# Kernel optimization log

Hardware: AMD Instinct MI355X
Metric: run time of the kernel (lower is better)

## Reference

```python
import jax, jax.numpy as jnp
import numpy as np

KK_THRESHOLD = 1000.0

def setup_inputs() -> dict:
    key = jax.random.key(0)
    k1, k2 = jax.random.split(key)
    x = jax.random.normal(k1, (8192, 4096), dtype=jnp.float32)
    # kernel initialized Uniform(-0.1, 0.1) as in the original layer
    kernel = jax.random.uniform(k2, (4096, 4096), dtype=jnp.float32, minval=-0.1, maxval=0.1)
    bias = jnp.zeros((4096,), dtype=jnp.float32)
    nmk = jnp.float32(1.0)
    kk = jnp.float32(1.0)  # < 1000 -> soft tanh quantization branch
    return {"x": x, "kernel": kernel, "bias": bias, "nmk": nmk, "kk": kk}

def reference(x, kernel, bias, nmk, kk):
    def soft(_):
        # training-time soft binarization: tanh(kk * W)
        return nmk * jnp.matmul(x, jnp.tanh(kernel * kk)) + bias
    def hard(_):
        # fully binarized: sign(W)
        return nmk * jnp.matmul(x, jnp.sign(kernel)) + bias
    return jax.lax.cond(kk < KK_THRESHOLD, soft, hard, operand=None)
```

## Files before the change

kernel.cpp:

```cpp
#include <hip/hip_runtime.h>
#include <hip/hip_bf16.h>
#include <stdint.h>

typedef __bf16 bf16x8 __attribute__((ext_vector_type(8)));
typedef float f32x4 __attribute__((ext_vector_type(4)));
typedef unsigned int u32;
typedef __attribute__((address_space(1))) const u32 g_u32;
typedef __attribute__((address_space(3))) u32 l_u32;

__device__ __forceinline__ unsigned short f32_bf16_rne(float f) {
    unsigned u = __float_as_uint(f);
    u += 0x7FFFu + ((u >> 16) & 1u);
    return (unsigned short)(u >> 16);
}

__device__ __forceinline__ float fast_tanh(float z) {
    return 1.0f - 2.0f / (1.0f + __expf(2.0f * z));
}

__device__ __forceinline__ void lds16(const void* g, void* l) {
    __builtin_amdgcn_global_load_lds((g_u32*)g, (l_u32*)l, 16, 0, 0);
}

__global__ __launch_bounds__(256) void prep(
    const float* __restrict__ x, unsigned short* __restrict__ xb, int n8,
    const float* __restrict__ W, unsigned short* __restrict__ Wt,
    const float* __restrict__ kk_p, int K, int N, int qbx, int qblocks)
{
    const int t = threadIdx.x;
    if ((int)blockIdx.x < qblocks) {
        __shared__ unsigned short tileT[64][66];
        const float kk = *kk_p;
        const bool soft = kk < 1000.0f;
        const int nb = (blockIdx.x % qbx) * 64;
        const int kb = (blockIdx.x / qbx) * 64;
#pragma unroll
        for (int j = 0; j < 4; ++j) {
            const int r  = j * 16 + (t >> 4);
            const int c4 = (t & 15) * 4;
            float4 w = *(const float4*)&W[(size_t)(kb + r) * N + nb + c4];
            float q0, q1, q2, q3;
            if (soft) {
                q0 = fast_tanh(w.x * kk); q1 = fast_tanh(w.y * kk);
                q2 = fast_tanh(w.z * kk); q3 = fast_tanh(w.w * kk);
            } else {
                q0 = (w.x > 0.f) ? 1.f : (w.x < 0.f ? -1.f : 0.f);
                q1 = (w.y > 0.f) ? 1.f : (w.y < 0.f ? -1.f : 0.f);
                q2 = (w.z > 0.f) ? 1.f : (w.z < 0.f ? -1.f : 0.f);
                q3 = (w.w > 0.f) ? 1.f : (w.w < 0.f ? -1.f : 0.f);
            }
            tileT[c4 + 0][r] = f32_bf16_rne(q0);
            tileT[c4 + 1][r] = f32_bf16_rne(q1);
            tileT[c4 + 2][r] = f32_bf16_rne(q2);
            tileT[c4 + 3][r] = f32_bf16_rne(q3);
        }
        __syncthreads();
#pragma unroll
        for (int j = 0; j < 2; ++j) {
            const int n = j * 32 + (t >> 3);
            const int c = (t & 7) * 8;
            uint4 v;
            v.x = *(const u32*)&tileT[n][c + 0];
            v.y = *(const u32*)&tileT[n][c + 2];
            v.z = *(const u32*)&tileT[n][c + 4];
            v.w = *(const u32*)&tileT[n][c + 6];
            *(uint4*)&Wt[(size_t)(nb + n) * K + kb + c] = v;
        }
    } else {
        const int i = ((int)blockIdx.x - qblocks) * 256 + t;
        if (i >= n8) return;
        const float4* p = (const float4*)x + (size_t)i * 2;
        float4 a = p[0];
        float4 b = p[1];
        union { unsigned short u[8]; uint4 v; } o;
        o.u[0] = f32_bf16_rne(a.x); o.u[1] = f32_bf16_rne(a.y);
        o.u[2] = f32_bf16_rne(a.z); o.u[3] = f32_bf16_rne(a.w);
        o.u[4] = f32_bf16_rne(b.x); o.u[5] = f32_bf16_rne(b.y);
        o.u[6] = f32_bf16_rne(b.z); o.u[7] = f32_bf16_rne(b.w);
        *((uint4*)xb + i) = o.v;
    }
}

__global__ __launch_bounds__(512, 2) void gemm_bf16_256(
    const unsigned short* __restrict__ A,
    const unsigned short* __restrict__ Bt,
    const float* __restrict__ bias,
    const float* __restrict__ nmk_p,
    float* __restrict__ C,
    int M, int N, int K)
{
    __shared__ __align__(16) char lds[131072];

    const int tid  = threadIdx.x;
    const int wave = tid >> 6;
    const int lane = tid & 63;
    const int wr = wave >> 2;
    const int wc = wave & 3;

    const int nbx = N >> 8;
    const int nwg = (int)gridDim.x;
    int id = (int)blockIdx.x;
    {
        const int xcd = id & 7, lid = id >> 3;
        const int q8 = nwg >> 3, r8 = nwg & 7;
        id = (xcd < r8 ? xcd * (q8 + 1) : r8 * (q8 + 1) + (xcd - r8) * q8) + lid;
    }
    const int mTile = (id / nbx) << 8;
    const int nTile = (id % nbx) << 8;

    const size_t Kb = (size_t)K * 2;
    const char* pA[2];
    const char* pB[2];
#pragma unroll
    for (int q = 0; q < 2; ++q) {
        const int s  = (wave * 2 + q) * 64 + lane;
        const int g  = s >> 6;
        const int r4 = (s >> 2) & 15;
        const int c4 = (s & 3) ^ ((r4 >> 1) & 3);
        const int row = ((g >> 1) << 4) + r4;
        const int cb  = (((g & 1) << 2) + c4) << 4;
        pA[q] = (const char*)A  + (size_t)(mTile + row) * Kb + cb;
        pB[q] = (const char*)Bt + (size_t)(nTile + row) * Kb + cb;
    }
    const size_t HSTEP = (size_t)128 * Kb;
    const int w2k = wave * 2048;

    const int laneoff = ((lane & 15) << 6)
                      + ((((lane >> 4) ^ (((lane & 15) >> 1) & 3))) << 4);

    f32x4 acc[8][4] = {};
    const int NT = K >> 6;

#define STG_A(buf, t, h) do {                                                  \
    char* _d = lds + (buf) * 65536 + (h) * 16384 + w2k;                        \
    lds16(pA[0] + (size_t)(h) * HSTEP + (size_t)(t) * 128, _d);                \
    lds16(pA[1] + (size_t)(h) * HSTEP + (size_t)(t) * 128, _d + 1024);         \
} while (0)
#define STG_B(buf, t, h) do {                                                  \
    char* _d = lds + 32768 + (buf) * 65536 + (h) * 16384 + w2k;                \
    lds16(pB[0] + (size_t)(h) * HSTEP + (size_t)(t) * 128, _d);                \
    lds16(pB[1] + (size_t)(h) * HSTEP + (size_t)(t) * 128, _d + 1024);         \
} while (0)
#define LDA(dst, buf, mi, ks) dst = *(const bf16x8*)(lds + (buf) * 65536       \
        + ((wr * 8 + (mi)) * 2048) + (ks) * 1024 + laneoff)
#define LDB(dst, buf, ni, ks) dst = *(const bf16x8*)(lds + 32768               \
        + (buf) * 65536 + ((wc * 4 + (ni)) * 2048) + (ks) * 1024 + laneoff)
#define BAR() __builtin_amdgcn_s_barrier()
#define LGKM0() asm volatile("s_waitcnt lgkmcnt(0)" ::: "memory")
#define MFMA_Q(p)                                                              \
    __builtin_amdgcn_s_setprio(1);                                             \
    { _Pragma("unroll")                                                        \
      for (int ii = 0; ii < 2; ++ii) {                                         \
        _Pragma("unroll")                                                      \
        for (int ni = 0; ni < 4; ++ni) {                                       \
          _Pragma("unroll")                                                    \
          for (int ks = 0; ks < 2; ++ks)                                       \
            acc[2 * (p) + ii][ni] = __builtin_amdgcn_mfma_f32_16x16x32_bf16(   \
                af[ii][ks], bf[ni][ks], acc[2 * (p) + ii][ni], 0, 0, 0);       \
        } } }                                                                  \
    __builtin_amdgcn_s_setprio(0)

    STG_A(0, 0, 0); STG_A(0, 0, 1);
    STG_B(0, 0, 0); STG_B(0, 0, 1);
    STG_B(1, 1, 0); STG_B(1, 1, 1);
    asm volatile("s_waitcnt vmcnt(4)" ::: "memory");
    BAR();

    bf16x8 af[2][2], bf[4][2];

    for (int t = 0; t < NT; ++t) {
        const int buf = t & 1;
        const int tA = (t + 1 < NT) ? (t + 1) : 0;
        int tB = t + 2; if (tB >= NT) tB -= NT;

        LDB(bf[0][0], buf, 0, 0); LDB(bf[0][1], buf, 0, 1);
        LDB(bf[1][0], buf, 1, 0); LDB(bf[1][1], buf, 1, 1);
        LDB(bf[2][0], buf, 2, 0); LDB(bf[2][1], buf, 2, 1);
        LDB(bf[3][0], buf, 3, 0); LDB(bf[3][1], buf, 3, 1);
        LDA(af[0][0], buf, 0, 0); LDA(af[0][1], buf, 0, 1);
        LDA(af[1][0], buf, 1, 0); LDA(af[1][1], buf, 1, 1);
        STG_A(buf ^ 1, tA, 0);
        BAR(); LGKM0();
        MFMA_Q(0);
        BAR();

        LDA(af[0][0], buf, 2, 0); LDA(af[0][1], buf, 2, 1);
        LDA(af[1][0], buf, 3, 0); LDA(af[1][1], buf, 3, 1);
        STG_A(buf ^ 1, tA, 1);
        BAR(); LGKM0();
        MFMA_Q(1);
        BAR();

        LDA(af[0][0], buf, 4, 0); LDA(af[0][1], buf, 4, 1);
        LDA(af[1][0], buf, 5, 0); LDA(af[1][1], buf, 5, 1);
        STG_B(buf, tB, 0);
        BAR(); LGKM0();
        MFMA_Q(2);
        BAR();

        LDA(af[0][0], buf, 6, 0); LDA(af[0][1], buf, 6, 1);
        LDA(af[1][0], buf, 7, 0); LDA(af[1][1], buf, 7, 1);
        STG_B(buf, tB, 1);
        asm volatile("s_waitcnt vmcnt(4)" ::: "memory");
        BAR(); LGKM0();
        MFMA_Q(3);
        BAR();
    }

    const float nmk = *nmk_p;
    const int l15 = lane & 15, lh = lane >> 4;
    float bn[4];
#pragma unroll
    for (int ni = 0; ni < 4; ++ni) bn[ni] = bias[nTile + wc * 64 + ni * 16 + l15];

#pragma unroll
    for (int mi = 0; mi < 8; ++mi) {
        const int rbase = mTile + wr * 128 + mi * 16 + lh * 4;
#pragma unroll
        for (int ni = 0; ni < 4; ++ni) {
            const int col = nTile + wc * 64 + ni * 16 + l15;
#pragma unroll
            for (int reg = 0; reg < 4; ++reg) {
                C[(size_t)(rbase + reg) * N + col] = nmk * acc[mi][ni][reg] + bn[ni];
            }
        }
    }
#undef STG_A
#undef STG_B
#undef LDA
#undef LDB
#undef BAR
#undef LGKM0
#undef MFMA_Q
}

__global__ void fallback_gemm(const float* __restrict__ x, const float* __restrict__ W,
                              const float* __restrict__ bias, const float* __restrict__ nmk_p,
                              const float* __restrict__ kk_p, float* __restrict__ C,
                              int M, int N, int K) {
    __shared__ float At[16][17];
    __shared__ float Bq[16][17];
    const int tx = threadIdx.x, ty = threadIdx.y;
    const int n = blockIdx.x * 16 + tx;
    const int m = blockIdx.y * 16 + ty;
    const float kk = *kk_p;
    const bool soft = kk < 1000.f;
    float acc = 0.f;
    for (int k0 = 0; k0 < K; k0 += 16) {
        At[ty][tx] = x[(size_t)m * K + k0 + tx];
        float w = W[(size_t)(k0 + ty) * N + n];
        Bq[ty][tx] = soft ? tanhf(w * kk) : (w > 0.f ? 1.f : (w < 0.f ? -1.f : 0.f));
        __syncthreads();
#pragma unroll
        for (int kk2 = 0; kk2 < 16; ++kk2) acc += At[ty][kk2] * Bq[kk2][tx];
        __syncthreads();
    }
    C[(size_t)m * N + n] = (*nmk_p) * acc + bias[n];
}

extern "C" void kernel_launch(void* const* d_in, const int* in_sizes, int n_in,
                              void* d_out, int out_size, void* d_ws, size_t ws_size,
                              hipStream_t stream) {
    const float* x    = (const float*)d_in[0];
    const float* W    = (const float*)d_in[1];
    const float* bias = (const float*)d_in[2];
    const float* nmk  = (const float*)d_in[3];
    const float* kk   = (const float*)d_in[4];
    float* out = (float*)d_out;

    const int N = in_sizes[2];
    const int K = in_sizes[1] / N;
    const int M = in_sizes[0] / K;

    const size_t need = ((size_t)M * K + (size_t)N * K) * sizeof(unsigned short);
    const bool shapes_ok = (M % 256 == 0) && (N % 256 == 0) && (K % 64 == 0) &&
                           (K >= 128) && ((M * K) % 2048 == 0);

    if (ws_size >= need && shapes_ok) {
        unsigned short* xb = (unsigned short*)d_ws;
        unsigned short* Wt = xb + (size_t)M * K;

        const int n8 = (M * K) / 8;
        const int qbx = N / 64;
        const int qblocks = qbx * (K / 64);
        const int cblocks = (n8 + 255) / 256;
        prep<<<qblocks + cblocks, 256, 0, stream>>>(x, xb, n8, W, Wt, kk, K, N, qbx, qblocks);

        const int nwg = (M / 256) * (N / 256);
        gemm_bf16_256<<<nwg, 512, 0, stream>>>(xb, Wt, bias, nmk, out, M, N, K);
    } else {
        dim3 fg(N / 16, M / 16);
        fallback_gemm<<<fg, dim3(16, 16), 0, stream>>>(x, W, bias, nmk, kk, out, M, N, K);
    }
}
```

Measured before the change: 486.9 us.

## Switch GEMM to 32x32x16 MFMA tiles and split prep into separate kernels

The GEMM inner loop now uses 32x32x16 bf16 MFMA instructions with 16-wide accumulators instead of 16x16x32. This cuts the phases per K-step from four to two and changes the LDS fragment addressing and epilogue row mapping to match. The larger MFMA is meant to get more math per LDS read and fewer barriers, at the cost of a different register layout and larger staging batches per phase. The fused prep kernel is also split into separate x-conversion and weight-quantization kernels, with the x conversion reworked to 4 floats per thread and two segments per block.

New measurement: 524.8 us. 1.08x slower.

```diff
diff --git a/kernel.cpp b/kernel.cpp
--- a/kernel.cpp
+++ b/kernel.cpp
@@ -3,7 +3,7 @@
 #include <stdint.h>
 
 typedef __bf16 bf16x8 __attribute__((ext_vector_type(8)));
-typedef float f32x4 __attribute__((ext_vector_type(4)));
+typedef float f32x16 __attribute__((ext_vector_type(16)));
 typedef unsigned int u32;
 typedef __attribute__((address_space(1))) const u32 g_u32;
 typedef __attribute__((address_space(3))) u32 l_u32;
@@ -22,62 +22,65 @@
     __builtin_amdgcn_global_load_lds((g_u32*)g, (l_u32*)l, 16, 0, 0);
 }
 
-__global__ __launch_bounds__(256) void prep(
-    const float* __restrict__ x, unsigned short* __restrict__ xb, int n8,
+__global__ __launch_bounds__(256) void prep_w(
     const float* __restrict__ W, unsigned short* __restrict__ Wt,
-    const float* __restrict__ kk_p, int K, int N, int qbx, int qblocks)
+    const float* __restrict__ kk_p, int K, int N, int qbx)
 {
     const int t = threadIdx.x;
-    if ((int)blockIdx.x < qblocks) {
-        __shared__ unsigned short tileT[64][66];
-        const float kk = *kk_p;
-        const bool soft = kk < 1000.0f;
-        const int nb = (blockIdx.x % qbx) * 64;
-        const int kb = (blockIdx.x / qbx) * 64;
-#pragma unroll
-        for (int j = 0; j < 4; ++j) {
-            const int r  = j * 16 + (t >> 4);
-            const int c4 = (t & 15) * 4;
-            float4 w = *(const float4*)&W[(size_t)(kb + r) * N + nb + c4];
-            float q0, q1, q2, q3;
-            if (soft) {
-                q0 = fast_tanh(w.x * kk); q1 = fast_tanh(w.y * kk);
-                q2 = fast_tanh(w.z * kk); q3 = fast_tanh(w.w * kk);
-            } else {
-                q0 = (w.x > 0.f) ? 1.f : (w.x < 0.f ? -1.f : 0.f);
-                q1 = (w.y > 0.f) ? 1.f : (w.y < 0.f ? -1.f : 0.f);
-                q2 = (w.z > 0.f) ? 1.f : (w.z < 0.f ? -1.f : 0.f);
-                q3 = (w.w > 0.f) ? 1.f : (w.w < 0.f ? -1.f : 0.f);
-            }
-            tileT[c4 + 0][r] = f32_bf16_rne(q0);
-            tileT[c4 + 1][r] = f32_bf16_rne(q1);
-            tileT[c4 + 2][r] = f32_bf16_rne(q2);
-            tileT[c4 + 3][r] = f32_bf16_rne(q3);
+    __shared__ unsigned short tileT[64][66];
+    const float kk = *kk_p;
+    const bool soft = kk < 1000.0f;
+    const int nb = (blockIdx.x % qbx) * 64;
+    const int kb = (blockIdx.x / qbx) * 64;
+#pragma unroll
+    for (int j = 0; j < 4; ++j) {
+        const int r  = j * 16 + (t >> 4);
+        const int c4 = (t & 15) * 4;
+        float4 w = *(const float4*)&W[(size_t)(kb + r) * N + nb + c4];
+        float q0, q1, q2, q3;
+        if (soft) {
+            q0 = fast_tanh(w.x * kk); q1 = fast_tanh(w.y * kk);
+            q2 = fast_tanh(w.z * kk); q3 = fast_tanh(w.w * kk);
+        } else {
+            q0 = (w.x > 0.f) ? 1.f : (w.x < 0.f ? -1.f : 0.f);
+            q1 = (w.y > 0.f) ? 1.f : (w.y < 0.f ? -1.f : 0.f);
+            q2 = (w.z > 0.f) ? 1.f : (w.z < 0.f ? -1.f : 0.f);
+            q3 = (w.w > 0.f) ? 1.f : (w.w < 0.f ? -1.f : 0.f);
         }
-        __syncthreads();
-#pragma unroll
-        for (int j = 0; j < 2; ++j) {
-            const int n = j * 32 + (t >> 3);
-            const int c = (t & 7) * 8;
-            uint4 v;
-            v.x = *(const u32*)&tileT[n][c + 0];
-            v.y = *(const u32*)&tileT[n][c + 2];
-            v.z = *(const u32*)&tileT[n][c + 4];
-            v.w = *(const u32*)&tileT[n][c + 6];
-            *(uint4*)&Wt[(size_t)(nb + n) * K + kb + c] = v;
+        tileT[c4 + 0][r] = f32_bf16_rne(q0);
+        tileT[c4 + 1][r] = f32_bf16_rne(q1);
+        tileT[c4 + 2][r] = f32_bf16_rne(q2);
+        tileT[c4 + 3][r] = f32_bf16_rne(q3);
+    }
+    __syncthreads();
+#pragma unroll
+    for (int j = 0; j < 2; ++j) {
+        const int n = j * 32 + (t >> 3);
+        const int c = (t & 7) * 8;
+        uint4 v;
+        v.x = *(const u32*)&tileT[n][c + 0];
+        v.y = *(const u32*)&tileT[n][c + 2];
+        v.z = *(const u32*)&tileT[n][c + 4];
+        v.w = *(const u32*)&tileT[n][c + 6];
+        *(uint4*)&Wt[(size_t)(nb + n) * K + kb + c] = v;
+    }
+}
+
+__global__ __launch_bounds__(256) void prep_x(
+    const float* __restrict__ x, unsigned short* __restrict__ xb, int nfloat)
+{
+    const int base = (int)blockIdx.x * 2048;
+    const int t = threadIdx.x;
+#pragma unroll
+    for (int seg = 0; seg < 2; ++seg) {
+        const int i = base + seg * 1024 + t * 4;
+        if (i < nfloat) {
+            float4 a = *(const float4*)(x + i);
+            u32 lo = (u32)f32_bf16_rne(a.x) | ((u32)f32_bf16_rne(a.y) << 16);
+            u32 hi = (u32)f32_bf16_rne(a.z) | ((u32)f32_bf16_rne(a.w) << 16);
+            uint2 o; o.x = lo; o.y = hi;
+            *(uint2*)(xb + i) = o;
         }
-    } else {
-        const int i = ((int)blockIdx.x - qblocks) * 256 + t;
-        if (i >= n8) return;
-        const float4* p = (const float4*)x + (size_t)i * 2;
-        float4 a = p[0];
-        float4 b = p[1];
-        union { unsigned short u[8]; uint4 v; } o;
-        o.u[0] = f32_bf16_rne(a.x); o.u[1] = f32_bf16_rne(a.y);
-        o.u[2] = f32_bf16_rne(a.z); o.u[3] = f32_bf16_rne(a.w);
-        o.u[4] = f32_bf16_rne(b.x); o.u[5] = f32_bf16_rne(b.y);
-        o.u[6] = f32_bf16_rne(b.z); o.u[7] = f32_bf16_rne(b.w);
-        *((uint4*)xb + i) = o.v;
     }
 }
 
@@ -125,10 +128,15 @@
     const size_t HSTEP = (size_t)128 * Kb;
     const int w2k = wave * 2048;
 
-    const int laneoff = ((lane & 15) << 6)
-                      + ((((lane >> 4) ^ (((lane & 15) >> 1) & 3))) << 4);
-
-    f32x4 acc[8][4] = {};
+    const int lrow = lane & 31, lr4 = lrow & 15, lg = lrow >> 4, lhi = lane >> 5;
+    const int swz = (lr4 >> 1) & 3;
+    int loff[4];
+#pragma unroll
+    for (int s = 0; s < 4; ++s)
+        loff[s] = lg * 2048 + (s >> 1) * 1024 + lr4 * 64
+                + (((((s & 1) << 1) | lhi) ^ swz) << 4);
+
+    f32x16 acc[4][2] = {};
     const int NT = K >> 6;
 
 #define STG_A(buf, t, h) do {                                                  \
@@ -141,10 +149,10 @@
     lds16(pB[0] + (size_t)(h) * HSTEP + (size_t)(t) * 128, _d);                \
     lds16(pB[1] + (size_t)(h) * HSTEP + (size_t)(t) * 128, _d + 1024);         \
 } while (0)
-#define LDA(dst, buf, mi, ks) dst = *(const bf16x8*)(lds + (buf) * 65536       \
-        + ((wr * 8 + (mi)) * 2048) + (ks) * 1024 + laneoff)
-#define LDB(dst, buf, ni, ks) dst = *(const bf16x8*)(lds + 32768               \
-        + (buf) * 65536 + ((wc * 4 + (ni)) * 2048) + (ks) * 1024 + laneoff)
+#define LDA32(dst, buf, mi, s) dst = *(const bf16x8*)(lds + (buf) * 65536      \
+        + wr * 16384 + (mi) * 4096 + loff[s])
+#define LDB32(dst, buf, ni, s) dst = *(const bf16x8*)(lds + 32768              \
+        + (buf) * 65536 + wc * 8192 + (ni) * 4096 + loff[s])
 #define BAR() __builtin_amdgcn_s_barrier()
 #define LGKM0() asm volatile("s_waitcnt lgkmcnt(0)" ::: "memory")
 #define MFMA_Q(p)                                                              \
@@ -152,11 +160,11 @@
     { _Pragma("unroll")                                                        \
       for (int ii = 0; ii < 2; ++ii) {                                         \
         _Pragma("unroll")                                                      \
-        for (int ni = 0; ni < 4; ++ni) {                                       \
+        for (int ni = 0; ni < 2; ++ni) {                                       \
           _Pragma("unroll")                                                    \
-          for (int ks = 0; ks < 2; ++ks)                                       \
-            acc[2 * (p) + ii][ni] = __builtin_amdgcn_mfma_f32_16x16x32_bf16(   \
-                af[ii][ks], bf[ni][ks], acc[2 * (p) + ii][ni], 0, 0, 0);       \
+          for (int s = 0; s < 4; ++s)                                          \
+            acc[2 * (p) + ii][ni] = __builtin_amdgcn_mfma_f32_32x32x16_bf16(   \
+                af[ii][s], bf[ni][s], acc[2 * (p) + ii][ni], 0, 0, 0);         \
         } } }                                                                  \
     __builtin_amdgcn_s_setprio(0)
 
@@ -166,69 +174,61 @@
     asm volatile("s_waitcnt vmcnt(4)" ::: "memory");
     BAR();
 
-    bf16x8 af[2][2], bf[4][2];
+    bf16x8 af[2][4], bf[2][4];
 
     for (int t = 0; t < NT; ++t) {
         const int buf = t & 1;
         const int tA = (t + 1 < NT) ? (t + 1) : 0;
         int tB = t + 2; if (tB >= NT) tB -= NT;
 
-        LDB(bf[0][0], buf, 0, 0); LDB(bf[0][1], buf, 0, 1);
-        LDB(bf[1][0], buf, 1, 0); LDB(bf[1][1], buf, 1, 1);
-        LDB(bf[2][0], buf, 2, 0); LDB(bf[2][1], buf, 2, 1);
-        LDB(bf[3][0], buf, 3, 0); LDB(bf[3][1], buf, 3, 1);
-        LDA(af[0][0], buf, 0, 0); LDA(af[0][1], buf, 0, 1);
-        LDA(af[1][0], buf, 1, 0); LDA(af[1][1], buf, 1, 1);
+        LDB32(bf[0][0], buf, 0, 0); LDB32(bf[0][1], buf, 0, 1);
+        LDB32(bf[0][2], buf, 0, 2); LDB32(bf[0][3], buf, 0, 3);
+        LDB32(bf[1][0], buf, 1, 0); LDB32(bf[1][1], buf, 1, 1);
+        LDB32(bf[1][2], buf, 1, 2); LDB32(bf[1][3], buf, 1, 3);
+        LDA32(af[0][0], buf, 0, 0); LDA32(af[0][1], buf, 0, 1);
+        LDA32(af[0][2], buf, 0, 2); LDA32(af[0][3], buf, 0, 3);
+        LDA32(af[1][0], buf, 1, 0); LDA32(af[1][1], buf, 1, 1);
+        LDA32(af[1][2], buf, 1, 2); LDA32(af[1][3], buf, 1, 3);
         STG_A(buf ^ 1, tA, 0);
+        STG_A(buf ^ 1, tA, 1);
         BAR(); LGKM0();
         MFMA_Q(0);
         BAR();
 
-        LDA(af[0][0], buf, 2, 0); LDA(af[0][1], buf, 2, 1);
-        LDA(af[1][0], buf, 3, 0); LDA(af[1][1], buf, 3, 1);
-        STG_A(buf ^ 1, tA, 1);
+        LDA32(af[0][0], buf, 2, 0); LDA32(af[0][1], buf, 2, 1);
+        LDA32(af[0][2], buf, 2, 2); LDA32(af[0][3], buf, 2, 3);
+        LDA32(af[1][0], buf, 3, 0); LDA32(af[1][1], buf, 3, 1);
+        LDA32(af[1][2], buf, 3, 2); LDA32(af[1][3], buf, 3, 3);
+        STG_B(buf, tB, 0);
+        STG_B(buf, tB, 1);
         BAR(); LGKM0();
         MFMA_Q(1);
+        asm volatile("s_waitcnt vmcnt(4)" ::: "memory");
         BAR();
-
-        LDA(af[0][0], buf, 4, 0); LDA(af[0][1], buf, 4, 1);
-        LDA(af[1][0], buf, 5, 0); LDA(af[1][1], buf, 5, 1);
-        STG_B(buf, tB, 0);
-        BAR(); LGKM0();
-        MFMA_Q(2);
-        BAR();
-
-        LDA(af[0][0], buf, 6, 0); LDA(af[0][1], buf, 6, 1);
-        LDA(af[1][0], buf, 7, 0); LDA(af[1][1], buf, 7, 1);
-        STG_B(buf, tB, 1);
-        asm volatile("s_waitcnt vmcnt(4)" ::: "memory");
-        BAR(); LGKM0();
-        MFMA_Q(3);
-        BAR();
     }
 
     const float nmk = *nmk_p;
-    const int l15 = lane & 15, lh = lane >> 4;
-    float bn[4];
-#pragma unroll
-    for (int ni = 0; ni < 4; ++ni) bn[ni] = bias[nTile + wc * 64 + ni * 16 + l15];
-
-#pragma unroll
-    for (int mi = 0; mi < 8; ++mi) {
-        const int rbase = mTile + wr * 128 + mi * 16 + lh * 4;
-#pragma unroll
-        for (int ni = 0; ni < 4; ++ni) {
-            const int col = nTile + wc * 64 + ni * 16 + l15;
-#pragma unroll
-            for (int reg = 0; reg < 4; ++reg) {
-                C[(size_t)(rbase + reg) * N + col] = nmk * acc[mi][ni][reg] + bn[ni];
+    float bn[2];
+#pragma unroll
+    for (int ni = 0; ni < 2; ++ni) bn[ni] = bias[nTile + wc * 64 + ni * 32 + lrow];
+
+#pragma unroll
+    for (int mi = 0; mi < 4; ++mi) {
+        const int rbase = mTile + wr * 128 + mi * 32 + 4 * lhi;
+#pragma unroll
+        for (int ni = 0; ni < 2; ++ni) {
+            const int col = nTile + wc * 64 + ni * 32 + lrow;
+#pragma unroll
+            for (int reg = 0; reg < 16; ++reg) {
+                const int row = rbase + (reg & 3) + 8 * (reg >> 2);
+                C[(size_t)row * N + col] = nmk * acc[mi][ni][reg] + bn[ni];
             }
         }
     }
 #undef STG_A
 #undef STG_B
-#undef LDA
-#undef LDB
+#undef LDA32
+#undef LDB32
 #undef BAR
 #undef LGKM0
 #undef MFMA_Q
@@ -280,11 +280,13 @@
         unsigned short* xb = (unsigned short*)d_ws;
         unsigned short* Wt = xb + (size_t)M * K;
 
-        const int n8 = (M * K) / 8;
+        const int nfloat = M * K;
+        const int xblocks = (nfloat + 2047) / 2048;
         const int qbx = N / 64;
-        const int qblocks = qbx * (K / 64);
-        const int cblocks = (n8 + 255) / 256;
-        prep<<<qblocks + cblocks, 256, 0, stream>>>(x, xb, n8, W, Wt, kk, K, N, qbx, qblocks);
+        const int wblocks = qbx * (K / 64);
+
+        prep_x<<<xblocks, 256, 0, stream>>>(x, xb, nfloat);
+        prep_w<<<wblocks, 256, 0, stream>>>(W, Wt, kk, K, N, qbx);
 
         const int nwg = (M / 256) * (N / 256);
         gemm_bf16_256<<<nwg, 512, 0, stream>>>(xb, Wt, bias, nmk, out, M, N, K);
```

## Cut GEMM main-loop barriers and split prep into separate x and W kernels

Applied to the files above, without the earlier changes.

The GEMM main loop drops from eight workgroup barriers per K-step to two. Both halves of the next A tile are issued before the first MFMA quarter, and both halves of the B prefetch before the third, so global-to-LDS staging overlaps more compute. Explicit lgkmcnt waits are replaced by compiler memory fences around the barriers, leaving the compiler to insert LDS waits. The fused prep kernel is also split into separate x-conversion and W-quantization kernels, and x conversion now uses float4 loads with uint2 stores per thread. The risk is correctness of LDS reuse with fewer barriers, plus the overhead of one extra kernel launch.

Result: slower. 505.9 us (+3.9%).

```diff
diff --git a/kernel.cpp b/kernel.cpp
--- a/kernel.cpp
+++ b/kernel.cpp
@@ -22,62 +22,65 @@
     __builtin_amdgcn_global_load_lds((g_u32*)g, (l_u32*)l, 16, 0, 0);
 }
 
-__global__ __launch_bounds__(256) void prep(
-    const float* __restrict__ x, unsigned short* __restrict__ xb, int n8,
+__global__ __launch_bounds__(256) void prep_w(
     const float* __restrict__ W, unsigned short* __restrict__ Wt,
-    const float* __restrict__ kk_p, int K, int N, int qbx, int qblocks)
+    const float* __restrict__ kk_p, int K, int N, int qbx)
 {
     const int t = threadIdx.x;
-    if ((int)blockIdx.x < qblocks) {
-        __shared__ unsigned short tileT[64][66];
-        const float kk = *kk_p;
-        const bool soft = kk < 1000.0f;
-        const int nb = (blockIdx.x % qbx) * 64;
-        const int kb = (blockIdx.x / qbx) * 64;
-#pragma unroll
-        for (int j = 0; j < 4; ++j) {
-            const int r  = j * 16 + (t >> 4);
-            const int c4 = (t & 15) * 4;
-            float4 w = *(const float4*)&W[(size_t)(kb + r) * N + nb + c4];
-            float q0, q1, q2, q3;
-            if (soft) {
-                q0 = fast_tanh(w.x * kk); q1 = fast_tanh(w.y * kk);
-                q2 = fast_tanh(w.z * kk); q3 = fast_tanh(w.w * kk);
-            } else {
-                q0 = (w.x > 0.f) ? 1.f : (w.x < 0.f ? -1.f : 0.f);
-                q1 = (w.y > 0.f) ? 1.f : (w.y < 0.f ? -1.f : 0.f);
-                q2 = (w.z > 0.f) ? 1.f : (w.z < 0.f ? -1.f : 0.f);
-                q3 = (w.w > 0.f) ? 1.f : (w.w < 0.f ? -1.f : 0.f);
-            }
-            tileT[c4 + 0][r] = f32_bf16_rne(q0);
-            tileT[c4 + 1][r] = f32_bf16_rne(q1);
-            tileT[c4 + 2][r] = f32_bf16_rne(q2);
-            tileT[c4 + 3][r] = f32_bf16_rne(q3);
+    __shared__ unsigned short tileT[64][66];
+    const float kk = *kk_p;
+    const bool soft = kk < 1000.0f;
+    const int nb = (blockIdx.x % qbx) * 64;
+    const int kb = (blockIdx.x / qbx) * 64;
+#pragma unroll
+    for (int j = 0; j < 4; ++j) {
+        const int r  = j * 16 + (t >> 4);
+        const int c4 = (t & 15) * 4;
+        float4 w = *(const float4*)&W[(size_t)(kb + r) * N + nb + c4];
+        float q0, q1, q2, q3;
+        if (soft) {
+            q0 = fast_tanh(w.x * kk); q1 = fast_tanh(w.y * kk);
+            q2 = fast_tanh(w.z * kk); q3 = fast_tanh(w.w * kk);
+        } else {
+            q0 = (w.x > 0.f) ? 1.f : (w.x < 0.f ? -1.f : 0.f);
+            q1 = (w.y > 0.f) ? 1.f : (w.y < 0.f ? -1.f : 0.f);
+            q2 = (w.z > 0.f) ? 1.f : (w.z < 0.f ? -1.f : 0.f);
+            q3 = (w.w > 0.f) ? 1.f : (w.w < 0.f ? -1.f : 0.f);
         }
-        __syncthreads();
-#pragma unroll
-        for (int j = 0; j < 2; ++j) {
-            const int n = j * 32 + (t >> 3);
-            const int c = (t & 7) * 8;
-            uint4 v;
-            v.x = *(const u32*)&tileT[n][c + 0];
-            v.y = *(const u32*)&tileT[n][c + 2];
-            v.z = *(const u32*)&tileT[n][c + 4];
-            v.w = *(const u32*)&tileT[n][c + 6];
-            *(uint4*)&Wt[(size_t)(nb + n) * K + kb + c] = v;
+        tileT[c4 + 0][r] = f32_bf16_rne(q0);
+        tileT[c4 + 1][r] = f32_bf16_rne(q1);
+        tileT[c4 + 2][r] = f32_bf16_rne(q2);
+        tileT[c4 + 3][r] = f32_bf16_rne(q3);
+    }
+    __syncthreads();
+#pragma unroll
+    for (int j = 0; j < 2; ++j) {
+        const int n = j * 32 + (t >> 3);
+        const int c = (t & 7) * 8;
+        uint4 v;
+        v.x = *(const u32*)&tileT[n][c + 0];
+        v.y = *(const u32*)&tileT[n][c + 2];
+        v.z = *(const u32*)&tileT[n][c + 4];
+        v.w = *(const u32*)&tileT[n][c + 6];
+        *(uint4*)&Wt[(size_t)(nb + n) * K + kb + c] = v;
+    }
+}
+
+__global__ __launch_bounds__(256) void prep_x(
+    const float* __restrict__ x, unsigned short* __restrict__ xb, int nfloat)
+{
+    const int base = (int)blockIdx.x * 2048;
+    const int t = threadIdx.x;
+#pragma unroll
+    for (int seg = 0; seg < 2; ++seg) {
+        const int i = base + seg * 1024 + t * 4;
+        if (i < nfloat) {
+            float4 a = *(const float4*)(x + i);
+            u32 lo = (u32)f32_bf16_rne(a.x) | ((u32)f32_bf16_rne(a.y) << 16);
+            u32 hi = (u32)f32_bf16_rne(a.z) | ((u32)f32_bf16_rne(a.w) << 16);
+            uint2 o; o.x = lo; o.y = hi;
+            *(uint2*)(xb + i) = o;
         }
-    } else {
-        const int i = ((int)blockIdx.x - qblocks) * 256 + t;
-        if (i >= n8) return;
-        const float4* p = (const float4*)x + (size_t)i * 2;
-        float4 a = p[0];
-        float4 b = p[1];
-        union { unsigned short u[8]; uint4 v; } o;
-        o.u[0] = f32_bf16_rne(a.x); o.u[1] = f32_bf16_rne(a.y);
-        o.u[2] = f32_bf16_rne(a.z); o.u[3] = f32_bf16_rne(a.w);
-        o.u[4] = f32_bf16_rne(b.x); o.u[5] = f32_bf16_rne(b.y);
-        o.u[6] = f32_bf16_rne(b.z); o.u[7] = f32_bf16_rne(b.w);
-        *((uint4*)xb + i) = o.v;
     }
 }
 
@@ -145,8 +148,8 @@
         + ((wr * 8 + (mi)) * 2048) + (ks) * 1024 + laneoff)
 #define LDB(dst, buf, ni, ks) dst = *(const bf16x8*)(lds + 32768               \
         + (buf) * 65536 + ((wc * 4 + (ni)) * 2048) + (ks) * 1024 + laneoff)
-#define BAR() __builtin_amdgcn_s_barrier()
-#define LGKM0() asm volatile("s_waitcnt lgkmcnt(0)" ::: "memory")
+#define CFENCE() asm volatile("" ::: "memory")
+#define BAR() do { CFENCE(); __builtin_amdgcn_s_barrier(); CFENCE(); } while (0)
 #define MFMA_Q(p)                                                              \
     __builtin_amdgcn_s_setprio(1);                                             \
     { _Pragma("unroll")                                                        \
@@ -180,30 +183,22 @@
         LDA(af[0][0], buf, 0, 0); LDA(af[0][1], buf, 0, 1);
         LDA(af[1][0], buf, 1, 0); LDA(af[1][1], buf, 1, 1);
         STG_A(buf ^ 1, tA, 0);
-        BAR(); LGKM0();
+        STG_A(buf ^ 1, tA, 1);
         MFMA_Q(0);
-        BAR();
-
         LDA(af[0][0], buf, 2, 0); LDA(af[0][1], buf, 2, 1);
         LDA(af[1][0], buf, 3, 0); LDA(af[1][1], buf, 3, 1);
-        STG_A(buf ^ 1, tA, 1);
-        BAR(); LGKM0();
         MFMA_Q(1);
         BAR();
 
         LDA(af[0][0], buf, 4, 0); LDA(af[0][1], buf, 4, 1);
         LDA(af[1][0], buf, 5, 0); LDA(af[1][1], buf, 5, 1);
         STG_B(buf, tB, 0);
-        BAR(); LGKM0();
+        STG_B(buf, tB, 1);
         MFMA_Q(2);
-        BAR();
-
         LDA(af[0][0], buf, 6, 0); LDA(af[0][1], buf, 6, 1);
         LDA(af[1][0], buf, 7, 0); LDA(af[1][1], buf, 7, 1);
-        STG_B(buf, tB, 1);
+        MFMA_Q(3);
         asm volatile("s_waitcnt vmcnt(4)" ::: "memory");
-        BAR(); LGKM0();
-        MFMA_Q(3);
         BAR();
     }
 
@@ -230,7 +225,7 @@
 #undef LDA
 #undef LDB
 #undef BAR
-#undef LGKM0
+#undef CFENCE
 #undef MFMA_Q
 }
 
@@ -280,11 +275,13 @@
         unsigned short* xb = (unsigned short*)d_ws;
         unsigned short* Wt = xb + (size_t)M * K;
 
-        const int n8 = (M * K) / 8;
+        const int nfloat = M * K;
+        const int xblocks = (nfloat + 2047) / 2048;
         const int qbx = N / 64;
-        const int qblocks = qbx * (K / 64);
-        const int cblocks = (n8 + 255) / 256;
-        prep<<<qblocks + cblocks, 256, 0, stream>>>(x, xb, n8, W, Wt, kk, K, N, qbx, qblocks);
+        const int wblocks = qbx * (K / 64);
+
+        prep_x<<<xblocks, 256, 0, stream>>>(x, xb, nfloat);
+        prep_w<<<wblocks, 256, 0, stream>>>(W, Wt, kk, K, N, qbx);
 
         const int nwg = (M / 256) * (N / 256);
         gemm_bf16_256<<<nwg, 512, 0, stream>>>(xb, Wt, bias, nmk, out, M, N, K);
```
